# Optimization experiments

Measured on AMD Instinct MI355X. Metric: run time of the kernel, lower is better.

## Reference

```python
import jax, jax.numpy as jnp
import numpy as np

B = 16          # number of point clouds (equal-sized, contiguous batch ids)
NC_PER = 1024   # coarse points per cloud
NF_PER = 4096   # fine points per cloud
K = 3           # knn_interpolate neighbors
C_IN = 512      # coarse feature channels
C_SKIP = 256    # skip feature channels
C_OUT = 512
BN_EPS = 1e-5


def setup_inputs() -> dict:
    key = jax.random.key(0)
    ks = jax.random.split(key, 8)
    Nc, Nf = B * NC_PER, B * NF_PER
    d_in = C_IN + C_SKIP
    x = jax.random.normal(ks[0], (Nc, C_IN), jnp.float32)
    pos = jax.random.uniform(ks[1], (Nc, 3), jnp.float32)
    batch = jnp.repeat(jnp.arange(B, dtype=jnp.int64), NC_PER)
    x_skip = jax.random.normal(ks[2], (Nf, C_SKIP), jnp.float32)
    pos_skip = jax.random.uniform(ks[3], (Nf, 3), jnp.float32)
    batch_skip = jnp.repeat(jnp.arange(B, dtype=jnp.int64), NF_PER)
    W1 = jax.random.normal(ks[4], (d_in, C_OUT), jnp.float32) / np.sqrt(d_in)
    W2 = jax.random.normal(ks[5], (C_OUT, C_OUT), jnp.float32) / np.sqrt(C_OUT)
    return {
        "x": x, "pos": pos, "batch": batch,
        "x_skip": x_skip, "pos_skip": pos_skip, "batch_skip": batch_skip,
        "W1": W1, "b1": jnp.zeros((C_OUT,), jnp.float32),
        "g1": jnp.ones((C_OUT,), jnp.float32), "be1": jnp.zeros((C_OUT,), jnp.float32),
        "W2": W2, "b2": jnp.zeros((C_OUT,), jnp.float32),
        "g2": jnp.ones((C_OUT,), jnp.float32), "be2": jnp.zeros((C_OUT,), jnp.float32),
    }


def _knn_interpolate(x, pos, pos_skip):
    # batches are contiguous and equal-sized -> reshape to [B, n, .] (honors batch/batch_skip)
    xb = x.reshape(B, NC_PER, C_IN)
    pc = pos.reshape(B, NC_PER, 3)
    pf = pos_skip.reshape(B, NF_PER, 3)
    # squared pairwise distances [B, NF_PER, NC_PER] via ||a||^2 + ||b||^2 - 2ab
    d2 = ((pf * pf).sum(-1)[:, :, None]
          + (pc * pc).sum(-1)[:, None, :]
          - 2.0 * jnp.einsum('bfd,bcd->bfc', pf, pc))
    neg_d2, idx = jax.lax.top_k(-d2, K)           # [B, NF_PER, K]
    w = 1.0 / jnp.maximum(-neg_d2, 1e-16)         # inverse squared-distance weights
    gathered = jax.vmap(lambda xi, ii: xi[ii])(xb, idx)   # [B, NF_PER, K, C_IN]
    y = (w[..., None] * gathered).sum(2) / w.sum(2)[..., None]
    return y.reshape(B * NF_PER, C_IN)


def _bn_act(h, g, be):
    # BatchNorm1d in training mode (biased variance) + ReLU
    mu = h.mean(0)
    var = ((h - mu) ** 2).mean(0)
    return jax.nn.relu((h - mu) * jax.lax.rsqrt(var + BN_EPS) * g + be)


def reference(x, pos, batch, x_skip, pos_skip, batch_skip,
              W1, b1, g1, be1, W2, b2, g2, be2):
    xi = _knn_interpolate(x, pos, pos_skip)        # [Nf, C_IN]
    h = jnp.concatenate([xi, x_skip], axis=1)      # [Nf, C_IN + C_SKIP]
    h = _bn_act(h @ W1 + b1, g1, be1)
    h = _bn_act(h @ W2 + b2, g2, be2)
    return (h, pos_skip, batch_skip)
```

## Files before the change

kernel.cpp:

```cpp
#include <hip/hip_runtime.h>
#include <cstdint>
#include <cstddef>

#define BATCHES   16
#define NC_PER    1024
#define NF_PER    4096
#define NC_TOT    (BATCHES * NC_PER)
#define NF_TOT    (BATCHES * NF_PER)
#define C_IN      512
#define C_SKIP    256
#define D_IN      (C_IN + C_SKIP)
#define C_OUT     512
#define BN_EPS    1e-5f

typedef __bf16 bf16x8 __attribute__((ext_vector_type(8)));
typedef __bf16 bf16x4 __attribute__((ext_vector_type(4)));
typedef float  f32x4  __attribute__((ext_vector_type(4)));

static_assert(sizeof(__bf16) == 2, "bf16 size");

__device__ __forceinline__ bf16x8 load16(const __bf16* p) {
  f32x4 r;
  asm volatile("global_load_dwordx4 %0, %1, off" : "=v"(r) : "v"(p));
  union { f32x4 f; bf16x8 b; } u; u.f = r; return u.b;
}

__global__ __launch_bounds__(256) void prep_kernel(
    const float* __restrict__ pos,
    const float* __restrict__ pos_skip,
    int4*  __restrict__ idx3,
    float4* __restrict__ w3,
    const float* __restrict__ W1, const float* __restrict__ W2,
    __bf16* __restrict__ W1t, __bf16* __restrict__ W2t)
{
  __shared__ float s_pos[NC_PER * 3];
  __shared__ float s_pc2[NC_PER];
  __shared__ float s_pd[4][64][3];
  __shared__ int   s_pi[4][64][3];

  const int tid = threadIdx.x;

  if (blockIdx.x >= 1024) {
    int idx = (blockIdx.x - 1024) * 256 + tid;
    if (idx < D_IN * C_OUT) {
      int n = idx / D_IN, k = idx - n * D_IN;
      W1t[idx] = (__bf16)W1[k * C_OUT + n];
    } else {
      idx -= D_IN * C_OUT;
      if (idx < C_OUT * C_OUT) {
        int n = idx >> 9, k = idx & 511;
        W2t[idx] = (__bf16)W2[k * C_OUT + n];
      }
    }
    return;
  }

  const int bi    = blockIdx.x;
  const int fbase = bi * 64;
  const int b     = fbase >> 12;
  const int cbase = b * NC_PER;

  for (int i = tid; i < NC_PER * 3; i += 256)
    s_pos[i] = pos[(size_t)cbase * 3 + i];
  __syncthreads();
  for (int j = tid; j < NC_PER; j += 256) {
    float cx = s_pos[j * 3 + 0], cy = s_pos[j * 3 + 1], cz = s_pos[j * 3 + 2];
    s_pc2[j] = __fadd_rn(__fadd_rn(__fmul_rn(cx, cx), __fmul_rn(cy, cy)),
                         __fmul_rn(cz, cz));
  }
  __syncthreads();

  const int p   = tid & 63;
  const int seg = tid >> 6;
  const int f   = fbase + p;
  const float px = pos_skip[f * 3 + 0];
  const float py = pos_skip[f * 3 + 1];
  const float pz = pos_skip[f * 3 + 2];
  const float pf2 = __fadd_rn(__fadd_rn(__fmul_rn(px, px), __fmul_rn(py, py)),
                              __fmul_rn(pz, pz));
  float b0 = 1e30f, b1 = 1e30f, b2 = 1e30f;
  int   i0 = 0,     i1 = 0,     i2 = 0;
  const int j0 = seg * 256;
#pragma unroll 4
  for (int jj = 0; jj < 256; ++jj) {
    const int j = j0 + jj;
    float cx = s_pos[j * 3 + 0], cy = s_pos[j * 3 + 1], cz = s_pos[j * 3 + 2];
    float dot = __fadd_rn(__fadd_rn(__fmul_rn(px, cx), __fmul_rn(py, cy)),
                          __fmul_rn(pz, cz));
    float d2 = __fsub_rn(__fadd_rn(pf2, s_pc2[j]), __fmul_rn(2.0f, dot));
    if (d2 < b2) {
      if (d2 < b1) {
        b2 = b1; i2 = i1;
        if (d2 < b0) { b1 = b0; i1 = i0; b0 = d2; i0 = j; }
        else         { b1 = d2; i1 = j; }
      } else { b2 = d2; i2 = j; }
    }
  }
  s_pd[seg][p][0] = b0; s_pd[seg][p][1] = b1; s_pd[seg][p][2] = b2;
  s_pi[seg][p][0] = i0; s_pi[seg][p][1] = i1; s_pi[seg][p][2] = i2;
  __syncthreads();

  if (tid < 64) {
    float m0 = 1e30f, m1 = 1e30f, m2 = 1e30f;
    int  mi0 = 0,    mi1 = 0,    mi2 = 0;
#pragma unroll
    for (int s = 0; s < 4; ++s)
#pragma unroll
      for (int k = 0; k < 3; ++k) {
        float d = s_pd[s][tid][k];
        int   i = s_pi[s][tid][k];
        if (d < m2 || (d == m2 && i < mi2)) {
          if (d < m1 || (d == m1 && i < mi1)) {
            m2 = m1; mi2 = mi1;
            if (d < m0 || (d == m0 && i < mi0)) {
              m1 = m0; mi1 = mi0; m0 = d; mi0 = i;
            } else { m1 = d; mi1 = i; }
          } else { m2 = d; mi2 = i; }
        }
      }
    float w0 = 1.0f / fmaxf(m0, 1e-16f);
    float w1 = 1.0f / fmaxf(m1, 1e-16f);
    float w2 = 1.0f / fmaxf(m2, 1e-16f);
    float inv = 1.0f / __fadd_rn(__fadd_rn(w0, w1), w2);
    const int fo = fbase + tid;
    idx3[fo] = make_int4(mi0, mi1, mi2, 0);
    w3[fo]   = make_float4(w0 * inv, w1 * inv, w2 * inv, 0.f);
  }
}

__global__ __launch_bounds__(256) void gather_interp(
    const float* __restrict__ x,
    const float* __restrict__ x_skip,
    const int4*  __restrict__ idx3,
    const float4* __restrict__ w3,
    __bf16* __restrict__ h0)
{
  const int bi   = blockIdx.x;
  const int xcd  = bi & 7;
  const int slot = bi >> 3;
  const int batch = xcd * 2 + (slot >> 10);
  const int blk   = slot & 1023;
  const int wv = threadIdx.x >> 6, ln = threadIdx.x & 63;
  const int f = batch * NF_PER + blk * 4 + wv;
  const int cbase = batch * NC_PER;

  const int4   id = idx3[f];
  const float4 w  = w3[f];
  const float* x0 = x + (size_t)(cbase + id.x) * C_IN;
  const float* x1 = x + (size_t)(cbase + id.y) * C_IN;
  const float* x2 = x + (size_t)(cbase + id.z) * C_IN;
  __bf16* o = h0 + (size_t)f * D_IN;
  const int c0 = ln * 4;
#pragma unroll
  for (int it = 0; it < 2; ++it) {
    const int c = c0 + it * 256;
    float4 a0 = *(const float4*)(x0 + c);
    float4 a1 = *(const float4*)(x1 + c);
    float4 a2 = *(const float4*)(x2 + c);
    bf16x4 ov;
    ov[0] = (__bf16)(w.x * a0.x + w.y * a1.x + w.z * a2.x);
    ov[1] = (__bf16)(w.x * a0.y + w.y * a1.y + w.z * a2.y);
    ov[2] = (__bf16)(w.x * a0.z + w.y * a1.z + w.z * a2.z);
    ov[3] = (__bf16)(w.x * a0.w + w.y * a1.w + w.z * a2.w);
    *(bf16x4*)(o + c) = ov;
  }
  float4 s = *(const float4*)(x_skip + (size_t)f * C_SKIP + c0);
  bf16x4 sv;
  sv[0] = (__bf16)s.x; sv[1] = (__bf16)s.y;
  sv[2] = (__bf16)s.z; sv[3] = (__bf16)s.w;
  *(bf16x4*)(o + C_IN + c0) = sv;
}

template <int K, bool FUSE_BN>
__global__ __launch_bounds__(512, 2) void gemm_bt(
    const __bf16* __restrict__ A,
    const __bf16* __restrict__ Bt,
    const float*  __restrict__ bias,
    __bf16* __restrict__ Cout,
    float* __restrict__ part1,
    const float* __restrict__ ab)
{
  constexpr int NT = K / 64;
  __shared__ __align__(16) __bf16 As[2 * 16384];
  __shared__ __align__(16) __bf16 Bs[2 * 16384];
  __shared__ float s_red[4][4][16][2];
  __shared__ float s_ab[1024];

  const int tid  = threadIdx.x;
  const int wave = tid >> 6, lane = tid & 63;
  const int quad = lane >> 4, l16 = lane & 15;
  const int wm = wave >> 2, wn = wave & 3;

  const int bid  = blockIdx.x;
  const int work = (bid & 7) * 64 + (bid >> 3);
  const int mt = work >> 1, nt = work & 1;
  const int m0 = mt * 256, n0 = nt * 256;

  const int slot = lane & 7, rsub = lane >> 3;
  const int rowA = wave * 8 + rsub;
  const int kSw  = (slot ^ rsub) * 8;
  const int ldsChunkBase = (wave * 64) * 8;

  auto stage_half = [&](const __bf16* __restrict__ src, int rowBase, int t,
                        __bf16* dst) {
#pragma unroll
    for (int q = 0; q < 2; ++q) {
      __builtin_amdgcn_global_load_lds(
          (const __attribute__((address_space(1))) unsigned int*)(
              src + (size_t)(rowBase + q * 64 + rowA) * K + t * 64 + kSw),
          (__attribute__((address_space(3))) unsigned int*)(
              dst + q * 4096 + ldsChunkBase),
          16, 0, 0);
    }
  };

  bf16x8 ar[4];

  auto load_a_regs = [&](int tt) {
#pragma unroll
    for (int h = 0; h < 2; ++h)
#pragma unroll
      for (int q = 0; q < 2; ++q)
        ar[h * 2 + q] = load16(A + (size_t)(m0 + h * 128 + q * 64 + rowA) * K +
                               tt * 64 + slot * 8);
  };
  auto bn_write_A = [&](int tt, __bf16* dstbuf) {
    const int cb = tt * 64 + slot * 8;
    const float4 aL = *(const float4*)&s_ab[cb];
    const float4 aH = *(const float4*)&s_ab[cb + 4];
    const float4 bL = *(const float4*)&s_ab[512 + cb];
    const float4 bH = *(const float4*)&s_ab[512 + cb + 4];
#pragma unroll
    for (int i = 0; i < 4; ++i) {
      bf16x8 v = ar[i]; bf16x8 o;
      o[0] = (__bf16)fmaxf(fmaf((float)v[0], aL.x, bL.x), 0.f);
      o[1] = (__bf16)fmaxf(fmaf((float)v[1], aL.y, bL.y), 0.f);
      o[2] = (__bf16)fmaxf(fmaf((float)v[2], aL.z, bL.z), 0.f);
      o[3] = (__bf16)fmaxf(fmaf((float)v[3], aL.w, bL.w), 0.f);
      o[4] = (__bf16)fmaxf(fmaf((float)v[4], aH.x, bH.x), 0.f);
      o[5] = (__bf16)fmaxf(fmaf((float)v[5], aH.y, bH.y), 0.f);
      o[6] = (__bf16)fmaxf(fmaf((float)v[6], aH.z, bH.z), 0.f);
      o[7] = (__bf16)fmaxf(fmaf((float)v[7], aH.w, bH.w), 0.f);
      const int h = i >> 1, q = i & 1;
      *(bf16x8*)(dstbuf + h * 8192 + (size_t)(q * 64 + rowA) * 64 + kSw) = o;
    }
  };

  f32x4 acc[8][4] = {};
  const int swz  = (l16 & 7) << 3;
  const int brow = (wn & 1) * 64;

  if constexpr (FUSE_BN) {
    for (int i = tid; i < 1024; i += 512) s_ab[i] = ab[i];
    load_a_regs(0);
    stage_half(Bt, n0,       0, Bs);
    stage_half(Bt, n0 + 128, 0, Bs + 8192);
    __syncthreads();
    bn_write_A(0, As);
    asm volatile("s_waitcnt lgkmcnt(0)" ::: "memory");
    __builtin_amdgcn_sched_barrier(0);
    __builtin_amdgcn_s_barrier();
  } else {
    stage_half(A,  m0,       0, As);
    stage_half(Bt, n0,       0, Bs);
    stage_half(A,  m0 + 128, 0, As + 8192);
    stage_half(Bt, n0 + 128, 0, Bs + 8192);
  }

  bf16x8 aA[4][2], bB[4][2];
#pragma unroll 2
  for (int t = 0; t < NT; ++t) {
    const int cur = t & 1;
    const __bf16* Ab = As + (cur * 2 + wm) * 8192;
    const __bf16* Bb = Bs + (cur * 2 + (wn >> 1)) * 8192;
    __bf16* Asn = As + (cur ^ 1) * 16384;
    __bf16* Bsn = Bs + (cur ^ 1) * 16384;

    if (t + 1 < NT) {
      if constexpr (FUSE_BN) {
        load_a_regs(t + 1);
        stage_half(Bt, n0, t + 1, Bsn);
        asm volatile("s_waitcnt vmcnt(6)" ::: "memory");
      } else {
        stage_half(A,  m0, t + 1, Asn);
        stage_half(Bt, n0, t + 1, Bsn);
        asm volatile("s_waitcnt vmcnt(4)" ::: "memory");
      }
    } else {
      asm volatile("s_waitcnt vmcnt(0)" ::: "memory");
    }
    __builtin_amdgcn_sched_barrier(0);
    __builtin_amdgcn_s_barrier();
#pragma unroll
    for (int mf = 0; mf < 4; ++mf)
#pragma unroll
      for (int ks = 0; ks < 2; ++ks)
        aA[mf][ks] = *(const bf16x8*)(Ab + (mf * 16 + l16) * 64 +
                                      ((ks * 32 + quad * 8) ^ swz));
#pragma unroll
    for (int nf = 0; nf < 2; ++nf)
#pragma unroll
      for (int ks = 0; ks < 2; ++ks)
        bB[nf][ks] = *(const bf16x8*)(Bb + (brow + nf * 16 + l16) * 64 +
                                      ((ks * 32 + quad * 8) ^ swz));
    __builtin_amdgcn_s_setprio(1);
#pragma unroll
    for (int mf = 0; mf < 4; ++mf)
#pragma unroll
      for (int nf = 0; nf < 2; ++nf)
#pragma unroll
        for (int ks = 0; ks < 2; ++ks)
          acc[mf][nf] = __builtin_amdgcn_mfma_f32_16x16x32_bf16(
              aA[mf][ks], bB[nf][ks], acc[mf][nf], 0, 0, 0);
    __builtin_amdgcn_s_setprio(0);
    __builtin_amdgcn_s_barrier();

    if (t + 1 < NT) {
      stage_half(Bt, n0 + 128, t + 1, Bsn + 8192);
      if constexpr (!FUSE_BN)
        stage_half(A, m0 + 128, t + 1, Asn + 8192);
    }
#pragma unroll
    for (int nf = 2; nf < 4; ++nf)
#pragma unroll
      for (int ks = 0; ks < 2; ++ks)
        bB[nf][ks] = *(const bf16x8*)(Bb + (brow + nf * 16 + l16) * 64 +
                                      ((ks * 32 + quad * 8) ^ swz));
    __builtin_amdgcn_s_setprio(1);
#pragma unroll
    for (int mf = 0; mf < 4; ++mf)
#pragma unroll
      for (int nf = 2; nf < 4; ++nf)
#pragma unroll
        for (int ks = 0; ks < 2; ++ks)
          acc[mf][nf] = __builtin_amdgcn_mfma_f32_16x16x32_bf16(
              aA[mf][ks], bB[nf][ks], acc[mf][nf], 0, 0, 0);
    __builtin_amdgcn_s_setprio(0);
    __builtin_amdgcn_s_barrier();

#pragma unroll
    for (int mf = 0; mf < 4; ++mf)
#pragma unroll
      for (int ks = 0; ks < 2; ++ks)
        aA[mf][ks] = *(const bf16x8*)(Ab + (64 + mf * 16 + l16) * 64 +
                                      ((ks * 32 + quad * 8) ^ swz));
    __builtin_amdgcn_s_setprio(1);
#pragma unroll
    for (int mf = 0; mf < 4; ++mf)
#pragma unroll
      for (int nf = 0; nf < 2; ++nf)
#pragma unroll
        for (int ks = 0; ks < 2; ++ks)
          acc[4 + mf][nf] = __builtin_amdgcn_mfma_f32_16x16x32_bf16(
              aA[mf][ks], bB[nf][ks], acc[4 + mf][nf], 0, 0, 0);
    __builtin_amdgcn_s_setprio(0);
    __builtin_amdgcn_s_barrier();

    __builtin_amdgcn_s_setprio(1);
#pragma unroll
    for (int mf = 0; mf < 4; ++mf)
#pragma unroll
      for (int nf = 2; nf < 4; ++nf)
#pragma unroll
        for (int ks = 0; ks < 2; ++ks)
          acc[4 + mf][nf] = __builtin_amdgcn_mfma_f32_16x16x32_bf16(
              aA[mf][ks], bB[nf][ks], acc[4 + mf][nf], 0, 0, 0);
    __builtin_amdgcn_s_setprio(0);
    if constexpr (FUSE_BN) {
      if (t + 1 < NT) {
        asm volatile("s_waitcnt vmcnt(4)" ::: "memory");
        __builtin_amdgcn_sched_barrier(0);
        bn_write_A(t + 1, Asn);
        asm volatile("s_waitcnt lgkmcnt(0)" ::: "memory");
        __builtin_amdgcn_sched_barrier(0);
      }
    }
    __builtin_amdgcn_s_barrier();
  }

  float sArr[4], ssArr[4];
  {
    __bf16* cbase = wm ? Bs : As;
#pragma unroll
    for (int nf = 0; nf < 4; ++nf) {
      const int cl = wn * 64 + nf * 16 + l16;
      const float bv = bias[n0 + cl];
      float s = 0.f, ss = 0.f;
#pragma unroll
      for (int mf = 0; mf < 8; ++mf) {
        const int rl = (wm * 128 + mf * 16 + quad * 4) & 127;
#pragma unroll
        for (int r = 0; r < 4; ++r) {
          const float v = acc[mf][nf][r] + bv;
          s += v; ss += v * v;
          cbase[(rl + r) * 256 + (cl ^ (quad << 4))] = (__bf16)v;
        }
      }
      s  += __shfl_down(s, 32);  s  += __shfl_down(s, 16);
      ss += __shfl_down(ss, 32); ss += __shfl_down(ss, 16);
      sArr[nf] = s; ssArr[nf] = ss;
    }
  }
  if (wm == 1 && quad == 0) {
#pragma unroll
    for (int nf = 0; nf < 4; ++nf) {
      s_red[wn][nf][l16][0] = sArr[nf];
      s_red[wn][nf][l16][1] = ssArr[nf];
    }
  }
  __syncthreads();

#pragma unroll
  for (int p = 0; p < 16; ++p) {
    const int i   = p * 512 + tid;
    const int row = i >> 5;
    const int cc  = (i & 31) * 8;
    const __bf16* base = (p < 8) ? As : Bs;
    bf16x8 v = *(const bf16x8*)&base[(row & 127) * 256 +
                                     (cc ^ (((row >> 2) & 3) << 4))];
    *(bf16x8*)&Cout[(size_t)(m0 + row) * 512 + n0 + cc] = v;
  }

  if (wm == 0 && quad == 0) {
    float* rowp = part1 + (size_t)mt * 1024;
#pragma unroll
    for (int nf = 0; nf < 4; ++nf) {
      const int n = n0 + wn * 64 + nf * 16 + l16;
      rowp[n]       = sArr[nf]  + s_red[wn][nf][l16][0];
      rowp[512 + n] = ssArr[nf] + s_red[wn][nf][l16][1];
    }
  }
}

__global__ __launch_bounds__(256) void reduce_partials(
    const float* __restrict__ part1, float* __restrict__ part2) {
  const int rb = blockIdx.x;
  const int t  = threadIdx.x;
#pragma unroll
  for (int k = 0; k < 4; ++k) {
    const int c = k * 256 + t;
    float acc = 0.f;
    const float* p = part1 + (size_t)rb * 16 * 1024 + c;
#pragma unroll
    for (int r = 0; r < 16; ++r) { acc += *p; p += 1024; }
    part2[rb * 1024 + c] = acc;
  }
}

__global__ void finalize_stats(const float* __restrict__ part2,
                               const float* __restrict__ g,
                               const float* __restrict__ be,
                               float* __restrict__ ab, float invM) {
  const int c = blockIdx.x * 256 + threadIdx.x;
  if (c < 512) {
    float s = 0.f, ss = 0.f;
#pragma unroll
    for (int r = 0; r < 16; ++r) {
      s  += part2[r * 1024 + c];
      ss += part2[r * 1024 + 512 + c];
    }
    float mean = s * invM;
    float var  = ss * invM - mean * mean;
    float a = g[c] * rsqrtf(var + BN_EPS);
    ab[c] = a;
    ab[512 + c] = be[c] - mean * a;
  }
}

__global__ __launch_bounds__(256) void bnrelu_tail(
    const __bf16* __restrict__ H, const float* __restrict__ ab,
    float* __restrict__ O,
    const float* __restrict__ pos_skip, float* __restrict__ out2) {
  if (blockIdx.x >= 16384) {
    const int i = (blockIdx.x - 16384) * 256 + threadIdx.x;
    if (i < NF_TOT * 3) {
      out2[i] = pos_skip[i];
    } else {
      const int f = i - NF_TOT * 3;
      out2[i] = (float)(f >> 12);
    }
    return;
  }
  const size_t e = ((size_t)blockIdx.x * 256 + threadIdx.x) * 8;
  const int c = (int)(e & 511);
  bf16x8 h = *(const bf16x8*)(H + e);
  float4 o0, o1;
  o0.x = fmaxf(fmaf((float)h[0], ab[c + 0], ab[512 + c + 0]), 0.f);
  o0.y = fmaxf(fmaf((float)h[1], ab[c + 1], ab[512 + c + 1]), 0.f);
  o0.z = fmaxf(fmaf((float)h[2], ab[c + 2], ab[512 + c + 2]), 0.f);
  o0.w = fmaxf(fmaf((float)h[3], ab[c + 3], ab[512 + c + 3]), 0.f);
  o1.x = fmaxf(fmaf((float)h[4], ab[c + 4], ab[512 + c + 4]), 0.f);
  o1.y = fmaxf(fmaf((float)h[5], ab[c + 5], ab[512 + c + 5]), 0.f);
  o1.z = fmaxf(fmaf((float)h[6], ab[c + 6], ab[512 + c + 6]), 0.f);
  o1.w = fmaxf(fmaf((float)h[7], ab[c + 7], ab[512 + c + 7]), 0.f);
  *(float4*)(O + e)     = o0;
  *(float4*)(O + e + 4) = o1;
}

extern "C" void kernel_launch(void* const* d_in, const int* in_sizes, int n_in,
                              void* d_out, int out_size, void* d_ws, size_t ws_size,
                              hipStream_t stream) {
  (void)in_sizes; (void)n_in; (void)out_size; (void)ws_size;

  const float* x        = (const float*)d_in[0];
  const float* pos      = (const float*)d_in[1];
  const float* x_skip   = (const float*)d_in[3];
  const float* pos_skip = (const float*)d_in[4];
  const float* W1  = (const float*)d_in[6];
  const float* b1  = (const float*)d_in[7];
  const float* g1  = (const float*)d_in[8];
  const float* be1 = (const float*)d_in[9];
  const float* W2  = (const float*)d_in[10];
  const float* b2  = (const float*)d_in[11];
  const float* g2  = (const float*)d_in[12];
  const float* be2 = (const float*)d_in[13];
  float* out = (float*)d_out;

  char* ws = (char*)d_ws;
  __bf16* h0   = (__bf16*)(ws);
  __bf16* h2   = (__bf16*)(ws);
  __bf16* h1   = (__bf16*)(ws + 100663296ull);
  __bf16* W1t  = (__bf16*)(ws + 167772160ull);
  __bf16* W2t  = (__bf16*)(ws + 168558592ull);
  float*  ab1   = (float*)(ws + 169086976ull);
  float*  ab2   = (float*)(ws + 169095168ull);
  int4*   idx3  = (int4*)(ws + 169099264ull);
  float4* w3    = (float4*)(ws + 170147840ull);
  float*  part1 = (float*)(ws + 169099264ull);
  float*  part2 = (float*)(ws + 171196416ull);

  prep_kernel<<<1024 + (D_IN * C_OUT + C_OUT * C_OUT + 255) / 256, 256, 0, stream>>>(
      pos, pos_skip, idx3, w3, W1, W2, W1t, W2t);

  gather_interp<<<NF_TOT / 4, 256, 0, stream>>>(x, x_skip, idx3, w3, h0);

  gemm_bt<D_IN, false><<<512, 512, 0, stream>>>(h0, W1t, b1, h1, part1, nullptr);
  reduce_partials<<<16, 256, 0, stream>>>(part1, part2);
  finalize_stats<<<2, 256, 0, stream>>>(part2, g1, be1, ab1, 1.0f / (float)NF_TOT);

  gemm_bt<C_OUT, true><<<512, 512, 0, stream>>>(h1, W2t, b2, h2, part1, ab1);
  reduce_partials<<<16, 256, 0, stream>>>(part1, part2);
  finalize_stats<<<2, 256, 0, stream>>>(part2, g2, be2, ab2, 1.0f / (float)NF_TOT);

  bnrelu_tail<<<16384 + 1024, 256, 0, stream>>>(
      h2, ab2, out, pos_skip, out + (size_t)NF_TOT * 512);
}
```

Measured before the change: 462.8 us.

## Shrink GEMM tiles to 256x128 with K-step 32 for higher occupancy

Restructures the bf16 MFMA GEMM from 256x256 tiles with K-step 64 to 256x128 tiles with K-step 32. Each wave now owns a 64x64 sub-tile, and the grid doubles to 1024 blocks. Launch bounds go from 2 to 4 blocks per CU, using much smaller LDS buffers and a simpler single-phase loop. The aim is more blocks in flight and more latency hiding, at the cost of twice as many loop iterations and barriers and more re-reads of A from global memory. The epilogue now writes its output tile to LDS in two halves and reduces BN partial sums across four M-waves.

```diff
diff --git a/kernel.cpp b/kernel.cpp
--- a/kernel.cpp
+++ b/kernel.cpp
@@ -172,7 +172,7 @@
 }
 
 template <int K, bool FUSE_BN>
-__global__ __launch_bounds__(512, 2) void gemm_bt(
+__global__ __launch_bounds__(512, 4) void gemm_bt(
     const __bf16* __restrict__ A,
     const __bf16* __restrict__ Bt,
     const float*  __restrict__ bias,
@@ -180,59 +180,59 @@
     float* __restrict__ part1,
     const float* __restrict__ ab)
 {
-  constexpr int NT = K / 64;
-  __shared__ __align__(16) __bf16 As[2 * 16384];
-  __shared__ __align__(16) __bf16 Bs[2 * 16384];
-  __shared__ float s_red[4][4][16][2];
+  constexpr int NT = K / 32;
+  __shared__ __align__(16) __bf16 As[2][8192];
+  __shared__ __align__(16) __bf16 Bs[2][4096];
+  __shared__ float s_red[4][2][4][16][2];
   __shared__ float s_ab[1024];
 
   const int tid  = threadIdx.x;
   const int wave = tid >> 6, lane = tid & 63;
   const int quad = lane >> 4, l16 = lane & 15;
-  const int wm = wave >> 2, wn = wave & 3;
+  const int wm = wave >> 1, wn = wave & 1;
 
   const int bid  = blockIdx.x;
-  const int work = (bid & 7) * 64 + (bid >> 3);
-  const int mt = work >> 1, nt = work & 1;
-  const int m0 = mt * 256, n0 = nt * 256;
-
-  const int slot = lane & 7, rsub = lane >> 3;
-  const int rowA = wave * 8 + rsub;
-  const int kSw  = (slot ^ rsub) * 8;
-  const int ldsChunkBase = (wave * 64) * 8;
-
-  auto stage_half = [&](const __bf16* __restrict__ src, int rowBase, int t,
-                        __bf16* dst) {
-#pragma unroll
-    for (int q = 0; q < 2; ++q) {
+  const int work = (bid & 7) * 128 + (bid >> 3);
+  const int mt = work >> 2, nt = work & 3;
+  const int m0 = mt * 256, n0 = nt * 128;
+
+  const int srow  = tid >> 2;
+  const int colSw = (((tid & 3) ^ ((tid >> 3) & 3)) << 3);
+
+  auto stageA = [&](int t, int buf) {
+#pragma unroll
+    for (int p = 0; p < 2; ++p)
       __builtin_amdgcn_global_load_lds(
           (const __attribute__((address_space(1))) unsigned int*)(
-              src + (size_t)(rowBase + q * 64 + rowA) * K + t * 64 + kSw),
+              A + (size_t)(m0 + p * 128 + srow) * K + t * 32 + colSw),
           (__attribute__((address_space(3))) unsigned int*)(
-              dst + q * 4096 + ldsChunkBase),
+              &As[buf][p * 4096 + tid * 8]),
           16, 0, 0);
-    }
   };
-
-  bf16x8 ar[4];
-
-  auto load_a_regs = [&](int tt) {
-#pragma unroll
-    for (int h = 0; h < 2; ++h)
-#pragma unroll
-      for (int q = 0; q < 2; ++q)
-        ar[h * 2 + q] = load16(A + (size_t)(m0 + h * 128 + q * 64 + rowA) * K +
-                               tt * 64 + slot * 8);
+  auto stageB = [&](int t, int buf) {
+    __builtin_amdgcn_global_load_lds(
+        (const __attribute__((address_space(1))) unsigned int*)(
+            Bt + (size_t)(n0 + srow) * K + t * 32 + colSw),
+        (__attribute__((address_space(3))) unsigned int*)(
+            &Bs[buf][tid * 8]),
+        16, 0, 0);
   };
-  auto bn_write_A = [&](int tt, __bf16* dstbuf) {
-    const int cb = tt * 64 + slot * 8;
+
+  bf16x8 ar[2];
+  auto load_a_regs = [&](int t) {
+#pragma unroll
+    for (int p = 0; p < 2; ++p)
+      ar[p] = load16(A + (size_t)(m0 + p * 128 + srow) * K + t * 32 + colSw);
+  };
+  auto bn_write_A = [&](int t, int buf) {
+    const int cb = t * 32 + colSw;
     const float4 aL = *(const float4*)&s_ab[cb];
     const float4 aH = *(const float4*)&s_ab[cb + 4];
     const float4 bL = *(const float4*)&s_ab[512 + cb];
     const float4 bH = *(const float4*)&s_ab[512 + cb + 4];
 #pragma unroll
-    for (int i = 0; i < 4; ++i) {
-      bf16x8 v = ar[i]; bf16x8 o;
+    for (int p = 0; p < 2; ++p) {
+      bf16x8 v = ar[p]; bf16x8 o;
       o[0] = (__bf16)fmaxf(fmaf((float)v[0], aL.x, bL.x), 0.f);
       o[1] = (__bf16)fmaxf(fmaf((float)v[1], aL.y, bL.y), 0.f);
       o[2] = (__bf16)fmaxf(fmaf((float)v[2], aL.z, bL.z), 0.f);
@@ -241,136 +241,72 @@
       o[5] = (__bf16)fmaxf(fmaf((float)v[5], aH.y, bH.y), 0.f);
       o[6] = (__bf16)fmaxf(fmaf((float)v[6], aH.z, bH.z), 0.f);
       o[7] = (__bf16)fmaxf(fmaf((float)v[7], aH.w, bH.w), 0.f);
-      const int h = i >> 1, q = i & 1;
-      *(bf16x8*)(dstbuf + h * 8192 + (size_t)(q * 64 + rowA) * 64 + kSw) = o;
+      *(bf16x8*)&As[buf][p * 4096 + tid * 8] = o;
     }
   };
 
-  f32x4 acc[8][4] = {};
-  const int swz  = (l16 & 7) << 3;
-  const int brow = (wn & 1) * 64;
+  f32x4 acc[4][4] = {};
 
   if constexpr (FUSE_BN) {
     for (int i = tid; i < 1024; i += 512) s_ab[i] = ab[i];
     load_a_regs(0);
-    stage_half(Bt, n0,       0, Bs);
-    stage_half(Bt, n0 + 128, 0, Bs + 8192);
+    stageB(0, 0);
     __syncthreads();
-    bn_write_A(0, As);
+    bn_write_A(0, 0);
     asm volatile("s_waitcnt lgkmcnt(0)" ::: "memory");
     __builtin_amdgcn_sched_barrier(0);
     __builtin_amdgcn_s_barrier();
   } else {
-    stage_half(A,  m0,       0, As);
-    stage_half(Bt, n0,       0, Bs);
-    stage_half(A,  m0 + 128, 0, As + 8192);
-    stage_half(Bt, n0 + 128, 0, Bs + 8192);
-  }
-
-  bf16x8 aA[4][2], bB[4][2];
-#pragma unroll 2
+    stageA(0, 0);
+    stageB(0, 0);
+  }
+
   for (int t = 0; t < NT; ++t) {
     const int cur = t & 1;
-    const __bf16* Ab = As + (cur * 2 + wm) * 8192;
-    const __bf16* Bb = Bs + (cur * 2 + (wn >> 1)) * 8192;
-    __bf16* Asn = As + (cur ^ 1) * 16384;
-    __bf16* Bsn = Bs + (cur ^ 1) * 16384;
 
     if (t + 1 < NT) {
       if constexpr (FUSE_BN) {
         load_a_regs(t + 1);
-        stage_half(Bt, n0, t + 1, Bsn);
-        asm volatile("s_waitcnt vmcnt(6)" ::: "memory");
+        stageB(t + 1, cur ^ 1);
+        asm volatile("s_waitcnt vmcnt(3)" ::: "memory");
       } else {
-        stage_half(A,  m0, t + 1, Asn);
-        stage_half(Bt, n0, t + 1, Bsn);
-        asm volatile("s_waitcnt vmcnt(4)" ::: "memory");
+        stageA(t + 1, cur ^ 1);
+        stageB(t + 1, cur ^ 1);
+        asm volatile("s_waitcnt vmcnt(3)" ::: "memory");
       }
     } else {
       asm volatile("s_waitcnt vmcnt(0)" ::: "memory");
     }
     __builtin_amdgcn_sched_barrier(0);
     __builtin_amdgcn_s_barrier();
+
+    bf16x8 aA[4], bB[4];
+#pragma unroll
+    for (int mf = 0; mf < 4; ++mf) {
+      const int row = wm * 64 + mf * 16 + l16;
+      aA[mf] = *(const bf16x8*)&As[cur][row * 32 +
+                                        ((quad ^ ((row >> 1) & 3)) << 3)];
+    }
+#pragma unroll
+    for (int nf = 0; nf < 4; ++nf) {
+      const int row = wn * 64 + nf * 16 + l16;
+      bB[nf] = *(const bf16x8*)&Bs[cur][row * 32 +
+                                        ((quad ^ ((row >> 1) & 3)) << 3)];
+    }
+    __builtin_amdgcn_s_setprio(1);
 #pragma unroll
     for (int mf = 0; mf < 4; ++mf)
 #pragma unroll
-      for (int ks = 0; ks < 2; ++ks)
-        aA[mf][ks] = *(const bf16x8*)(Ab + (mf * 16 + l16) * 64 +
-                                      ((ks * 32 + quad * 8) ^ swz));
-#pragma unroll
-    for (int nf = 0; nf < 2; ++nf)
-#pragma unroll
-      for (int ks = 0; ks < 2; ++ks)
-        bB[nf][ks] = *(const bf16x8*)(Bb + (brow + nf * 16 + l16) * 64 +
-                                      ((ks * 32 + quad * 8) ^ swz));
-    __builtin_amdgcn_s_setprio(1);
-#pragma unroll
-    for (int mf = 0; mf < 4; ++mf)
-#pragma unroll
-      for (int nf = 0; nf < 2; ++nf)
-#pragma unroll
-        for (int ks = 0; ks < 2; ++ks)
-          acc[mf][nf] = __builtin_amdgcn_mfma_f32_16x16x32_bf16(
-              aA[mf][ks], bB[nf][ks], acc[mf][nf], 0, 0, 0);
+      for (int nf = 0; nf < 4; ++nf)
+        acc[mf][nf] = __builtin_amdgcn_mfma_f32_16x16x32_bf16(
+            aA[mf], bB[nf], acc[mf][nf], 0, 0, 0);
     __builtin_amdgcn_s_setprio(0);
-    __builtin_amdgcn_s_barrier();
-
-    if (t + 1 < NT) {
-      stage_half(Bt, n0 + 128, t + 1, Bsn + 8192);
-      if constexpr (!FUSE_BN)
-        stage_half(A, m0 + 128, t + 1, Asn + 8192);
-    }
-#pragma unroll
-    for (int nf = 2; nf < 4; ++nf)
-#pragma unroll
-      for (int ks = 0; ks < 2; ++ks)
-        bB[nf][ks] = *(const bf16x8*)(Bb + (brow + nf * 16 + l16) * 64 +
-                                      ((ks * 32 + quad * 8) ^ swz));
-    __builtin_amdgcn_s_setprio(1);
-#pragma unroll
-    for (int mf = 0; mf < 4; ++mf)
-#pragma unroll
-      for (int nf = 2; nf < 4; ++nf)
-#pragma unroll
-        for (int ks = 0; ks < 2; ++ks)
-          acc[mf][nf] = __builtin_amdgcn_mfma_f32_16x16x32_bf16(
-              aA[mf][ks], bB[nf][ks], acc[mf][nf], 0, 0, 0);
-    __builtin_amdgcn_s_setprio(0);
-    __builtin_amdgcn_s_barrier();
-
-#pragma unroll
-    for (int mf = 0; mf < 4; ++mf)
-#pragma unroll
-      for (int ks = 0; ks < 2; ++ks)
-        aA[mf][ks] = *(const bf16x8*)(Ab + (64 + mf * 16 + l16) * 64 +
-                                      ((ks * 32 + quad * 8) ^ swz));
-    __builtin_amdgcn_s_setprio(1);
-#pragma unroll
-    for (int mf = 0; mf < 4; ++mf)
-#pragma unroll
-      for (int nf = 0; nf < 2; ++nf)
-#pragma unroll
-        for (int ks = 0; ks < 2; ++ks)
-          acc[4 + mf][nf] = __builtin_amdgcn_mfma_f32_16x16x32_bf16(
-              aA[mf][ks], bB[nf][ks], acc[4 + mf][nf], 0, 0, 0);
-    __builtin_amdgcn_s_setprio(0);
-    __builtin_amdgcn_s_barrier();
-
-    __builtin_amdgcn_s_setprio(1);
-#pragma unroll
-    for (int mf = 0; mf < 4; ++mf)
-#pragma unroll
-      for (int nf = 2; nf < 4; ++nf)
-#pragma unroll
-        for (int ks = 0; ks < 2; ++ks)
-          acc[4 + mf][nf] = __builtin_amdgcn_mfma_f32_16x16x32_bf16(
-              aA[mf][ks], bB[nf][ks], acc[4 + mf][nf], 0, 0, 0);
-    __builtin_amdgcn_s_setprio(0);
+
     if constexpr (FUSE_BN) {
       if (t + 1 < NT) {
-        asm volatile("s_waitcnt vmcnt(4)" ::: "memory");
+        asm volatile("s_waitcnt vmcnt(1)" ::: "memory");
         __builtin_amdgcn_sched_barrier(0);
-        bn_write_A(t + 1, Asn);
+        bn_write_A(t + 1, cur ^ 1);
         asm volatile("s_waitcnt lgkmcnt(0)" ::: "memory");
         __builtin_amdgcn_sched_barrier(0);
       }
@@ -379,46 +315,59 @@
   }
 
   float sArr[4], ssArr[4];
-  {
-    __bf16* cbase = wm ? Bs : As;
+#pragma unroll
+  for (int nf = 0; nf < 4; ++nf) {
+    const float bv = bias[n0 + wn * 64 + nf * 16 + l16];
+    float s = 0.f, ss = 0.f;
+#pragma unroll
+    for (int mf = 0; mf < 4; ++mf)
+#pragma unroll
+      for (int r = 0; r < 4; ++r) {
+        const float v = acc[mf][nf][r] + bv;
+        s += v; ss += v * v;
+      }
+    s  += __shfl_down(s, 32);  s  += __shfl_down(s, 16);
+    ss += __shfl_down(ss, 32); ss += __shfl_down(ss, 16);
+    sArr[nf] = s; ssArr[nf] = ss;
+  }
+  if (quad == 0) {
 #pragma unroll
     for (int nf = 0; nf < 4; ++nf) {
-      const int cl = wn * 64 + nf * 16 + l16;
-      const float bv = bias[n0 + cl];
-      float s = 0.f, ss = 0.f;
-#pragma unroll
-      for (int mf = 0; mf < 8; ++mf) {
-        const int rl = (wm * 128 + mf * 16 + quad * 4) & 127;
-#pragma unroll
-        for (int r = 0; r < 4; ++r) {
-          const float v = acc[mf][nf][r] + bv;
-          s += v; ss += v * v;
-          cbase[(rl + r) * 256 + (cl ^ (quad << 4))] = (__bf16)v;
+      s_red[wm][wn][nf][l16][0] = sArr[nf];
+      s_red[wm][wn][nf][l16][1] = ssArr[nf];
+    }
+  }
+
+  __bf16* Aflat = &As[0][0];
+#pragma unroll
+  for (int r = 0; r < 2; ++r) {
+    __syncthreads();
+    if ((wm >> 1) == r) {
+      const int rbase = (wm & 1) * 64;
+#pragma unroll
+      for (int nf = 0; nf < 4; ++nf) {
+        const int cl = wn * 64 + nf * 16 + l16;
+        const float bv = bias[n0 + cl];
+        const int cw = cl ^ (quad << 4);
+#pragma unroll
+        for (int mf = 0; mf < 4; ++mf) {
+          const int rl = rbase + mf * 16 + quad * 4;
+#pragma unroll
+          for (int rr = 0; rr < 4; ++rr)
+            Aflat[(rl + rr) * 128 + cw] = (__bf16)(acc[mf][nf][rr] + bv);
         }
       }
-      s  += __shfl_down(s, 32);  s  += __shfl_down(s, 16);
-      ss += __shfl_down(ss, 32); ss += __shfl_down(ss, 16);
-      sArr[nf] = s; ssArr[nf] = ss;
-    }
-  }
-  if (wm == 1 && quad == 0) {
-#pragma unroll
-    for (int nf = 0; nf < 4; ++nf) {
-      s_red[wn][nf][l16][0] = sArr[nf];
-      s_red[wn][nf][l16][1] = ssArr[nf];
-    }
-  }
-  __syncthreads();
-
-#pragma unroll
-  for (int p = 0; p < 16; ++p) {
-    const int i   = p * 512 + tid;
-    const int row = i >> 5;
-    const int cc  = (i & 31) * 8;
-    const __bf16* base = (p < 8) ? As : Bs;
-    bf16x8 v = *(const bf16x8*)&base[(row & 127) * 256 +
-                                     (cc ^ (((row >> 2) & 3) << 4))];
-    *(bf16x8*)&Cout[(size_t)(m0 + row) * 512 + n0 + cc] = v;
+    }
+    __syncthreads();
+#pragma unroll
+    for (int p = 0; p < 4; ++p) {
+      const int i   = p * 512 + tid;
+      const int row = i >> 4;
+      const int cc  = (i & 15) * 8;
+      bf16x8 v = *(const bf16x8*)&Aflat[row * 128 +
+                                        (cc ^ (((row >> 2) & 3) << 4))];
+      *(bf16x8*)&Cout[(size_t)(m0 + r * 128 + row) * 512 + n0 + cc] = v;
+    }
   }
 
   if (wm == 0 && quad == 0) {
@@ -426,8 +375,14 @@
 #pragma unroll
     for (int nf = 0; nf < 4; ++nf) {
       const int n = n0 + wn * 64 + nf * 16 + l16;
-      rowp[n]       = sArr[nf]  + s_red[wn][nf][l16][0];
-      rowp[512 + n] = ssArr[nf] + s_red[wn][nf][l16][1];
+      float s = 0.f, ss = 0.f;
+#pragma unroll
+      for (int w = 0; w < 4; ++w) {
+        s  += s_red[w][wn][nf][l16][0];
+        ss += s_red[w][wn][nf][l16][1];
+      }
+      rowp[n]       = s;
+      rowp[512 + n] = ss;
     }
   }
 }
@@ -534,11 +489,11 @@
 
   gather_interp<<<NF_TOT / 4, 256, 0, stream>>>(x, x_skip, idx3, w3, h0);
 
-  gemm_bt<D_IN, false><<<512, 512, 0, stream>>>(h0, W1t, b1, h1, part1, nullptr);
+  gemm_bt<D_IN, false><<<1024, 512, 0, stream>>>(h0, W1t, b1, h1, part1, nullptr);
   reduce_partials<<<16, 256, 0, stream>>>(part1, part2);
   finalize_stats<<<2, 256, 0, stream>>>(part2, g1, be1, ab1, 1.0f / (float)NF_TOT);
 
-  gemm_bt<C_OUT, true><<<512, 512, 0, stream>>>(h1, W2t, b2, h2, part1, ab1);
+  gemm_bt<C_OUT, true><<<1024, 512, 0, stream>>>(h1, W2t, b2, h2, part1, ab1);
   reduce_partials<<<16, 256, 0, stream>>>(part1, part2);
   finalize_stats<<<2, 256, 0, stream>>>(part2, g2, be2, ab2, 1.0f / (float)NF_TOT);
 
```

Result: no change. 455.5 us (-1.6%).
